# Performance work log

Hardware: AMD Instinct MI355X
Metric: run time of the kernel (lower is better)

## Reference

```python
import jax, jax.numpy as jnp
import numpy as np

D_MODEL = 1024
N_HEADS = 16
D_K = D_MODEL // N_HEADS
FF_DIM = 4096
EPS = 1e-6
NEG = -1.0e9


def _layernorm(x, g, b):
    # torch: a_2 * (x - mean) / (std + eps) + b_2, std is unbiased (ddof=1)
    mean = jnp.mean(x, axis=-1, keepdims=True)
    std = jnp.std(x, axis=-1, keepdims=True, ddof=1)
    return g * (x - mean) / (std + EPS) + b


def setup_inputs() -> dict:
    key = jax.random.key(0)
    ks = jax.random.split(key, 8)
    s = 0.02
    x = jax.random.normal(ks[0], (2, 2048, D_MODEL), dtype=jnp.float32)
    mask = jnp.ones((2, 1, 1, 2048), dtype=jnp.int32)
    return {
        "x": x,
        "mask": mask,
        "wq": jax.random.normal(ks[1], (D_MODEL, D_MODEL), jnp.float32) * s,
        "wk": jax.random.normal(ks[2], (D_MODEL, D_MODEL), jnp.float32) * s,
        "wv": jax.random.normal(ks[3], (D_MODEL, D_MODEL), jnp.float32) * s,
        "wo": jax.random.normal(ks[4], (D_MODEL, D_MODEL), jnp.float32) * s,
        "bq": jnp.zeros((D_MODEL,), jnp.float32),
        "bk": jnp.zeros((D_MODEL,), jnp.float32),
        "bv": jnp.zeros((D_MODEL,), jnp.float32),
        "bo": jnp.zeros((D_MODEL,), jnp.float32),
        "w1": jax.random.normal(ks[5], (D_MODEL, FF_DIM), jnp.float32) * s,
        "b1": jnp.zeros((FF_DIM,), jnp.float32),
        "w2": jax.random.normal(ks[6], (FF_DIM, D_MODEL), jnp.float32) * s,
        "b2": jnp.zeros((D_MODEL,), jnp.float32),
        "ln1_g": jnp.ones((D_MODEL,), jnp.float32),
        "ln1_b": jnp.zeros((D_MODEL,), jnp.float32),
        "ln2_g": jnp.ones((D_MODEL,), jnp.float32),
        "ln2_b": jnp.zeros((D_MODEL,), jnp.float32),
    }


def reference(x, mask, wq, wk, wv, wo, bq, bk, bv, bo, w1, b1, w2, b2,
              ln1_g, ln1_b, ln2_g, ln2_b):
    B, S, _ = x.shape
    # --- sublayer 1: pre-norm self-attention with residual ---
    h = _layernorm(x, ln1_g, ln1_b)
    q = (h @ wq + bq).reshape(B, S, N_HEADS, D_K).transpose(0, 2, 1, 3)
    k = (h @ wk + bk).reshape(B, S, N_HEADS, D_K).transpose(0, 2, 1, 3)
    v = (h @ wv + bv).reshape(B, S, N_HEADS, D_K).transpose(0, 2, 1, 3)
    scores = jnp.einsum('bhqd,bhkd->bhqk', q, k) / np.sqrt(D_K).astype(np.float32)
    scores = jnp.where(mask == 0, NEG, scores)
    attn = jax.nn.softmax(scores, axis=-1)
    ctx = jnp.einsum('bhqk,bhkd->bhqd', attn, v)
    ctx = ctx.transpose(0, 2, 1, 3).reshape(B, S, D_MODEL)
    x = x + (ctx @ wo + bo)
    # --- sublayer 2: pre-norm FFN with residual ---
    h2 = _layernorm(x, ln2_g, ln2_b)
    ff = jax.nn.relu(h2 @ w1 + b1) @ w2 + b2
    return x + ff
```

## Files before the change

### kernel.cpp

```cpp
#include <hip/hip_runtime.h>

typedef unsigned short u16;
typedef unsigned int u32;
typedef __attribute__((ext_vector_type(8))) short bf16x8;
typedef __attribute__((ext_vector_type(4))) float f32x4;

__device__ __forceinline__ u16 f2bf(float f) {
  union { float f; unsigned int u; } x;
  x.f = f;
  unsigned int r = x.u + 0x7fffu + ((x.u >> 16) & 1u);
  return (u16)(r >> 16);
}

__device__ __forceinline__ float bf2f(u16 v) {
  union { unsigned int u; float f; } x;
  x.u = ((unsigned int)v) << 16;
  return x.f;
}

__device__ __forceinline__ u32 fbits(float f) {
  union { float f; u32 u; } x; x.f = f; return x.u;
}

__device__ __forceinline__ void async16(const u16* g, u16* l) {
  __builtin_amdgcn_global_load_lds((const __attribute__((address_space(1))) void*)g,
                                   (__attribute__((address_space(3))) void*)l, 16, 0, 0);
}

__device__ __forceinline__ void stage128x64(const u16* __restrict__ src, long row0, int k0,
                                            int ld, u16* lds, int wave, int lane) {
#pragma unroll
  for (int r = 0; r < 4; ++r) {
    int s = r * 256 + wave * 64 + lane;
    int row = s >> 3;
    int c = (s & 7) ^ (row & 7);
    async16(src + (row0 + row) * (long)ld + k0 + c * 8, lds + (r * 256 + wave * 64) * 8);
  }
}

__device__ __forceinline__ void stage_half512(const u16* __restrict__ src, long row0, int k0,
                                              int ld, u16* lbase, int wave, int lane) {
#pragma unroll
  for (int r = 0; r < 2; ++r) {
    int s = r * 512 + wave * 64 + lane;
    int row = s >> 3;
    int c = (s & 7) ^ (row & 7);
    async16(src + (row0 + row) * (long)ld + k0 + c * 8, lbase + (r * 512 + wave * 64) * 8);
  }
}

__device__ __forceinline__ void stage64x128(const u16* __restrict__ src, int col0, int ld,
                                            u16* lds, int wave, int lane) {
#pragma unroll
  for (int r = 0; r < 4; ++r) {
    int s = r * 256 + wave * 64 + lane;
    int row = s >> 4;
    int c = (s & 15) ^ (row & 15);
    async16(src + (long)row * ld + col0 + c * 8, lds + (r * 256 + wave * 64) * 8);
  }
}

__device__ __forceinline__ void ln_core(float4 v, const float* g, const float* b, int t,
                                        u16* outrow) {
  float s = v.x + v.y + v.z + v.w;
  float ss = v.x * v.x + v.y * v.y + v.z * v.z + v.w * v.w;
#pragma unroll
  for (int off = 32; off; off >>= 1) {
    s += __shfl_xor(s, off);
    ss += __shfl_xor(ss, off);
  }
  __shared__ float red[8];
  int wave = t >> 6, lane = t & 63;
  if (lane == 0) { red[wave] = s; red[wave + 4] = ss; }
  __syncthreads();
  float tot = red[0] + red[1] + red[2] + red[3];
  float tots = red[4] + red[5] + red[6] + red[7];
  float mean = tot * (1.0f / 1024.0f);
  float var = (tots - 1024.0f * mean * mean) * (1.0f / 1023.0f);
  var = fmaxf(var, 0.0f);
  float inv = 1.0f / (sqrtf(var) + 1e-6f);
  float4 gv = ((const float4*)g)[t];
  float4 bv = ((const float4*)b)[t];
  union { unsigned long long u64; u16 h[4]; } o;
  o.h[0] = f2bf(gv.x * (v.x - mean) * inv + bv.x);
  o.h[1] = f2bf(gv.y * (v.y - mean) * inv + bv.y);
  o.h[2] = f2bf(gv.z * (v.z - mean) * inv + bv.z);
  o.h[3] = f2bf(gv.w * (v.w - mean) * inv + bv.w);
  *(unsigned long long*)(outrow + t * 4) = o.u64;
}

__global__ __launch_bounds__(256) void prep(const float* __restrict__ wq,
                                            const float* __restrict__ wk,
                                            const float* __restrict__ wv,
                                            const float* __restrict__ wo,
                                            const float* __restrict__ w1,
                                            const float* __restrict__ w2,
                                            const float* __restrict__ x,
                                            const float* __restrict__ ln1_g,
                                            const float* __restrict__ ln1_b,
                                            u16* __restrict__ wqkvT,
                                            u16* __restrict__ w1T,
                                            u16* __restrict__ w2T,
                                            u16* __restrict__ hout) {
  const int bid = blockIdx.x;
  const int part = bid >> 12;
  const int local = bid & 4095;
  const int t = threadIdx.x;
  if (part == 1) {
    float4 v = ((const float4*)(x + (long)local * 1024))[t];
    ln_core(v, ln1_g, ln1_b, t, hout + (long)local * 1024);
    return;
  }
  __shared__ float tile[32][33];
  const float* src; u16* dst; int C, R, bx, by;
  if (part == 0) {
    int sub = local >> 10;
    src = sub == 0 ? wq : (sub == 1 ? wk : (sub == 2 ? wv : wo));
    dst = wqkvT + (long)sub * 1024 * 1024;
    C = 1024; R = 1024; bx = local & 31; by = (local >> 5) & 31;
  } else if (part == 2) {
    src = w1; dst = w1T; C = 4096; R = 1024; bx = local & 127; by = local >> 7;
  } else {
    src = w2; dst = w2T; C = 1024; R = 4096; bx = local & 31; by = local >> 5;
  }
  int c0 = bx * 32, r0 = by * 32;
  int tx = t & 31, ty = t >> 5;
#pragma unroll
  for (int i = 0; i < 32; i += 8)
    tile[ty + i][tx] = src[(long)(r0 + ty + i) * C + c0 + tx];
  __syncthreads();
#pragma unroll
  for (int i = 0; i < 32; i += 8)
    dst[(long)(c0 + ty + i) * R + r0 + tx] = f2bf(tile[tx][ty + i]);
}

__global__ __launch_bounds__(256) void ln_fuse(const float* __restrict__ x,
                                               const float* __restrict__ bres,
                                               const u16* __restrict__ p0,
                                               const u16* __restrict__ p1,
                                               const float* __restrict__ g,
                                               const float* __restrict__ b,
                                               float* __restrict__ yout,
                                               u16* __restrict__ hout) {
  int row = blockIdx.x, t = threadIdx.x;
  long base = (long)row * 1024;
  float4 xv = ((const float4*)(x + base))[t];
  float4 bo = ((const float4*)bres)[t];
  ushort4 a = ((const ushort4*)(p0 + base))[t];
  ushort4 c = ((const ushort4*)(p1 + base))[t];
  float4 y;
  y.x = xv.x + bo.x + bf2f(a.x) + bf2f(c.x);
  y.y = xv.y + bo.y + bf2f(a.y) + bf2f(c.y);
  y.z = xv.z + bo.z + bf2f(a.z) + bf2f(c.z);
  y.w = xv.w + bo.w + bf2f(a.w) + bf2f(c.w);
  ((float4*)(yout + base))[t] = y;
  ln_core(y, g, b, t, hout + base);
}

__global__ __launch_bounds__(256) void final_add(float* __restrict__ out,
                                                 const float* __restrict__ b2,
                                                 const u16* __restrict__ p0,
                                                 const u16* __restrict__ p1,
                                                 const u16* __restrict__ p2,
                                                 const u16* __restrict__ p3) {
  int row = blockIdx.x, t = threadIdx.x;
  long base = (long)row * 1024;
  float4 o = ((float4*)(out + base))[t];
  float4 bb = ((const float4*)b2)[t];
  ushort4 a = ((const ushort4*)(p0 + base))[t];
  ushort4 c = ((const ushort4*)(p1 + base))[t];
  ushort4 d = ((const ushort4*)(p2 + base))[t];
  ushort4 e = ((const ushort4*)(p3 + base))[t];
  o.x += bb.x + (bf2f(a.x) + bf2f(c.x)) + (bf2f(d.x) + bf2f(e.x));
  o.y += bb.y + (bf2f(a.y) + bf2f(c.y)) + (bf2f(d.y) + bf2f(e.y));
  o.z += bb.z + (bf2f(a.z) + bf2f(c.z)) + (bf2f(d.z) + bf2f(e.z));
  o.w += bb.w + (bf2f(a.w) + bf2f(c.w)) + (bf2f(d.w) + bf2f(e.w));
  ((float4*)(out + base))[t] = o;
}

template <int MODE>
__global__ __launch_bounds__(256) void gemm_bt(const u16* __restrict__ A,
                                               const u16* __restrict__ Bt, int M, int N, int K,
                                               void* __restrict__ outp,
                                               const float* __restrict__ bias0,
                                               const float* __restrict__ bias1,
                                               const float* __restrict__ bias2,
                                               u16* __restrict__ q_out, u16* __restrict__ k_out,
                                               u16* __restrict__ v_out) {
  __shared__ __align__(16) u16 lds[17408];
  u16* ldsA = lds;
  u16* ldsB = lds + 8192;
  const int tid = threadIdx.x;
  const int wave = tid >> 6, lane = tid & 63;
  const int lane16 = lane & 15, quad = lane >> 4;
  const int wm = (wave >> 1) * 64, wn = (wave & 1) * 64;
  const long m0 = (long)blockIdx.y * 128;
  const long n0 = (long)blockIdx.x * 128;
  const int kLen = K / gridDim.z;
  const int kBeg = blockIdx.z * kLen;

  const f32x4 fzero = {0.f, 0.f, 0.f, 0.f};
  f32x4 acc[4][4];
#pragma unroll
  for (int i = 0; i < 4; ++i)
#pragma unroll
    for (int j = 0; j < 4; ++j) acc[i][j] = fzero;

  for (int k0 = kBeg; k0 < kBeg + kLen; k0 += 64) {
    stage128x64(A, m0, k0, K, ldsA, wave, lane);
    stage128x64(Bt, n0, k0, K, ldsB, wave, lane);
    __syncthreads();
#pragma unroll
    for (int kk = 0; kk < 2; ++kk) {
      bf16x8 af[4], bfr[4];
#pragma unroll
      for (int i = 0; i < 4; ++i) {
        int row = wm + i * 16 + lane16;
        int c = (kk * 4 + quad) ^ (row & 7);
        af[i] = *(const bf16x8*)(ldsA + row * 64 + c * 8);
      }
#pragma unroll
      for (int j = 0; j < 4; ++j) {
        int row = wn + j * 16 + lane16;
        int c = (kk * 4 + quad) ^ (row & 7);
        bfr[j] = *(const bf16x8*)(ldsB + row * 64 + c * 8);
      }
#pragma unroll
      for (int i = 0; i < 4; ++i)
#pragma unroll
        for (int j = 0; j < 4; ++j)
          acc[i][j] = __builtin_amdgcn_mfma_f32_16x16x32_bf16(af[i], bfr[j], acc[i][j], 0, 0, 0);
    }
    __syncthreads();
  }

  if (MODE == 0 && (int)(n0 >> 10) == 2) {
#pragma unroll
    for (int j = 0; j < 4; ++j) {
      int lcol = wn + j * 16 + lane16;
      float bvj = bias2[(int)(n0 - 2048) + lcol];
#pragma unroll
      for (int i = 0; i < 4; ++i)
#pragma unroll
        for (int r = 0; r < 4; ++r) {
          int lrow = wm + i * 16 + quad * 4 + r;
          lds[lcol * 136 + lrow] = f2bf(acc[i][j][r] + bvj);
        }
    }
    __syncthreads();
    int lcol = tid >> 1, seg = tid & 1;
    int cc = (int)(n0 - 2048) + lcol;
    int head = cc >> 6, d = cc & 63;
    int bI = (int)(m0 >> 11), s0 = (int)(m0 & 2047);
    u16* dst = v_out + ((long)(bI * 16 + head) * 64 + d) * 2048 + s0 + seg * 64;
    const u16* s = lds + lcol * 136 + seg * 64;
#pragma unroll
    for (int c2 = 0; c2 < 8; ++c2) ((uint4*)dst)[c2] = ((const uint4*)s)[c2];
    return;
  }

  u16* pp = nullptr;
  if (MODE == 1) pp = blockIdx.z == 0 ? (u16*)outp : q_out;

#pragma unroll
  for (int j = 0; j < 4; ++j) {
    int col = (int)n0 + wn + j * 16 + lane16;
#pragma unroll
    for (int i = 0; i < 4; ++i) {
#pragma unroll
      for (int r = 0; r < 4; ++r) {
        int row = (int)m0 + wm + i * 16 + quad * 4 + r;
        float val = acc[i][j][r];
        if (MODE == 0) {
          int which = col >> 10, cc = col & 1023;
          float vv = val + (which == 0 ? bias0[cc] : bias1[cc]);
          int bb = row >> 11, sS = row & 2047, head = cc >> 6, d = cc & 63;
          long bh = (long)bb * 16 + head;
          if (which == 0) {
            q_out[(bh * 2048 + sS) * 64 + d] = f2bf(vv * 0.18033688f);
          } else {
            k_out[(bh * 2048 + sS) * 64 + d] = f2bf(vv);
          }
        } else if (MODE == 1) {
          pp[(long)row * N + col] = f2bf(val);
        }
      }
    }
  }
}

template <int MODE>
__global__ __launch_bounds__(512, 1) void gemm8(const u16* __restrict__ A,
                                                const u16* __restrict__ Bt, int M, int N, int K,
                                                void* __restrict__ outp,
                                                const float* __restrict__ bias) {
  __shared__ __align__(16) u16 lds[65536];
  (void)M;
  const int tid = threadIdx.x;
  const int wave = tid >> 6, lane = tid & 63;
  const int lane16 = lane & 15, quad = lane >> 4;
  const int wr2 = wave >> 2, wc2 = wave & 3;
  const long m0 = (long)blockIdx.y * 256;
  const long n0 = (long)blockIdx.x * 256;
  const int kLen = K / gridDim.z;
  const int kBeg = blockIdx.z * kLen;
  const int nT = kLen >> 6;

  u16* const ldsA = lds;
  u16* const ldsB = lds + 32768;

  const f32x4 fzero = {0.f, 0.f, 0.f, 0.f};
  f32x4 acc[2][2][4][2];
#pragma unroll
  for (int qa = 0; qa < 2; ++qa)
#pragma unroll
    for (int qb = 0; qb < 2; ++qb)
#pragma unroll
      for (int m = 0; m < 4; ++m)
#pragma unroll
        for (int n = 0; n < 2; ++n) acc[qa][qb][m][n] = fzero;

  stage_half512(A,  m0,       kBeg,      K, ldsA,                 wave, lane);
  stage_half512(Bt, n0,       kBeg,      K, ldsB,                 wave, lane);
  stage_half512(Bt, n0 + 128, kBeg,      K, ldsB + 8192,          wave, lane);
  stage_half512(A,  m0 + 128, kBeg,      K, ldsA + 8192,          wave, lane);
  stage_half512(A,  m0,       kBeg + 64, K, ldsA + 16384,         wave, lane);
  stage_half512(Bt, n0,       kBeg + 64, K, ldsB + 16384,         wave, lane);
  stage_half512(Bt, n0 + 128, kBeg + 64, K, ldsB + 16384 + 8192,  wave, lane);
  asm volatile("s_waitcnt vmcnt(10)" ::: "memory");
  asm volatile("s_barrier" ::: "memory");

  for (int t = 0; t < nT; ++t) {
    u16* const aB = ldsA + (t & 1) * 16384;
    u16* const bB = ldsB + (t & 1) * 16384;
    u16* const aN1 = ldsA + ((t + 1) & 1) * 16384;
    const int k1 = kBeg + (t + 1 < nT ? t + 1 : nT - 1) * 64;
    const int k2 = kBeg + (t + 2 < nT ? t + 2 : nT - 1) * 64;

    bf16x8 af[4][2], b0f[2][2], b1f[2][2];

#pragma unroll
    for (int m = 0; m < 4; ++m) {
      const int row = wr2 * 64 + m * 16 + lane16;
#pragma unroll
      for (int kk = 0; kk < 2; ++kk)
        af[m][kk] = *(const bf16x8*)(aB + row * 64 + (((kk * 4 + quad) ^ (row & 7)) << 3));
    }
#pragma unroll
    for (int n = 0; n < 2; ++n) {
      const int row = wc2 * 32 + n * 16 + lane16;
#pragma unroll
      for (int kk = 0; kk < 2; ++kk)
        b0f[n][kk] = *(const bf16x8*)(bB + row * 64 + (((kk * 4 + quad) ^ (row & 7)) << 3));
    }
    stage_half512(A, m0 + 128, k1, K, aN1 + 8192, wave, lane);
    asm volatile("s_barrier" ::: "memory");
    asm volatile("s_waitcnt lgkmcnt(0)" ::: "memory");
    __builtin_amdgcn_sched_barrier(0);
    __builtin_amdgcn_s_setprio(1);
#pragma unroll
    for (int m = 0; m < 4; ++m)
#pragma unroll
      for (int n = 0; n < 2; ++n) {
        acc[0][0][m][n] = __builtin_amdgcn_mfma_f32_16x16x32_bf16(af[m][0], b0f[n][0], acc[0][0][m][n], 0, 0, 0);
        acc[0][0][m][n] = __builtin_amdgcn_mfma_f32_16x16x32_bf16(af[m][1], b0f[n][1], acc[0][0][m][n], 0, 0, 0);
      }
    __builtin_amdgcn_s_setprio(0);
    asm volatile("s_waitcnt vmcnt(10)" ::: "memory");
    asm volatile("s_barrier" ::: "memory");

#pragma unroll
    for (int n = 0; n < 2; ++n) {
      const int row = 128 + wc2 * 32 + n * 16 + lane16;
#pragma unroll
      for (int kk = 0; kk < 2; ++kk)
        b1f[n][kk] = *(const bf16x8*)(bB + row * 64 + (((kk * 4 + quad) ^ (row & 7)) << 3));
    }
    stage_half512(A, m0, k2, K, aB, wave, lane);
    asm volatile("s_barrier" ::: "memory");
    asm volatile("s_waitcnt lgkmcnt(0)" ::: "memory");
    __builtin_amdgcn_sched_barrier(0);
    __builtin_amdgcn_s_setprio(1);
#pragma unroll
    for (int m = 0; m < 4; ++m)
#pragma unroll
      for (int n = 0; n < 2; ++n) {
        acc[0][1][m][n] = __builtin_amdgcn_mfma_f32_16x16x32_bf16(af[m][0], b1f[n][0], acc[0][1][m][n], 0, 0, 0);
        acc[0][1][m][n] = __builtin_amdgcn_mfma_f32_16x16x32_bf16(af[m][1], b1f[n][1], acc[0][1][m][n], 0, 0, 0);
      }
    __builtin_amdgcn_s_setprio(0);
    asm volatile("s_waitcnt vmcnt(10)" ::: "memory");
    asm volatile("s_barrier" ::: "memory");

#pragma unroll
    for (int m = 0; m < 4; ++m) {
      const int row = 128 + wr2 * 64 + m * 16 + lane16;
#pragma unroll
      for (int kk = 0; kk < 2; ++kk)
        af[m][kk] = *(const bf16x8*)(aB + row * 64 + (((kk * 4 + quad) ^ (row & 7)) << 3));
    }
    stage_half512(Bt, n0, k2, K, bB, wave, lane);
    asm volatile("s_barrier" ::: "memory");
    asm volatile("s_waitcnt lgkmcnt(0)" ::: "memory");
    __builtin_amdgcn_sched_barrier(0);
    __builtin_amdgcn_s_setprio(1);
#pragma unroll
    for (int m = 0; m < 4; ++m)
#pragma unroll
      for (int n = 0; n < 2; ++n) {
        acc[1][1][m][n] = __builtin_amdgcn_mfma_f32_16x16x32_bf16(af[m][0], b1f[n][0], acc[1][1][m][n], 0, 0, 0);
        acc[1][1][m][n] = __builtin_amdgcn_mfma_f32_16x16x32_bf16(af[m][1], b1f[n][1], acc[1][1][m][n], 0, 0, 0);
      }
    __builtin_amdgcn_s_setprio(0);
    asm volatile("s_waitcnt vmcnt(10)" ::: "memory");
    asm volatile("s_barrier" ::: "memory");

    stage_half512(Bt, n0 + 128, k2, K, bB + 8192, wave, lane);
    asm volatile("s_barrier" ::: "memory");
    __builtin_amdgcn_s_setprio(1);
#pragma unroll
    for (int m = 0; m < 4; ++m)
#pragma unroll
      for (int n = 0; n < 2; ++n) {
        acc[1][0][m][n] = __builtin_amdgcn_mfma_f32_16x16x32_bf16(af[m][0], b0f[n][0], acc[1][0][m][n], 0, 0, 0);
        acc[1][0][m][n] = __builtin_amdgcn_mfma_f32_16x16x32_bf16(af[m][1], b0f[n][1], acc[1][0][m][n], 0, 0, 0);
      }
    __builtin_amdgcn_s_setprio(0);
    asm volatile("s_waitcnt vmcnt(10)" ::: "memory");
    asm volatile("s_barrier" ::: "memory");
  }

  asm volatile("s_waitcnt vmcnt(0)" ::: "memory");

  if (MODE == 2) {
    u16* op = (u16*)outp;
#pragma unroll
    for (int qa = 0; qa < 2; ++qa)
#pragma unroll
      for (int qb = 0; qb < 2; ++qb)
#pragma unroll
        for (int n = 0; n < 2; ++n) {
          const int col = (int)n0 + qb * 128 + wc2 * 32 + n * 16 + lane16;
          const float bv = bias[col];
#pragma unroll
          for (int m = 0; m < 4; ++m) {
            const long rbase = ((long)m0 + qa * 128 + wr2 * 64 + m * 16 + quad * 4) * N + col;
#pragma unroll
            for (int r = 0; r < 4; ++r)
              op[rbase + (long)r * N] = f2bf(fmaxf(acc[qa][qb][m][n][r] + bv, 0.0f));
          }
        }
  } else {
    u16* pp = (u16*)outp + (long)blockIdx.z * 4194304;
#pragma unroll
    for (int qa = 0; qa < 2; ++qa)
#pragma unroll
      for (int qb = 0; qb < 2; ++qb)
#pragma unroll
        for (int n = 0; n < 2; ++n) {
          const int col = (int)n0 + qb * 128 + wc2 * 32 + n * 16 + lane16;
#pragma unroll
          for (int m = 0; m < 4; ++m) {
            const long rbase = ((long)m0 + qa * 128 + wr2 * 64 + m * 16 + quad * 4) * N + col;
#pragma unroll
            for (int r = 0; r < 4; ++r)
              pp[rbase + (long)r * N] = f2bf(acc[qa][qb][m][n][r]);
          }
        }
  }
}

#define FA_C0 28.854239f
__global__ __launch_bounds__(256) void flash_attn(const u16* __restrict__ q,
                                                  const u16* __restrict__ k,
                                                  const u16* __restrict__ v,
                                                  const int* __restrict__ mask,
                                                  u16* __restrict__ ctx) {
  const int fid = blockIdx.y * 16 + blockIdx.x;
  const int xcd = fid & 7, slot = fid >> 3;
  const int bh = xcd * 4 + (slot >> 4);
  const int q0 = (slot & 15) * 128;
  const int b = bh >> 4, h = bh & 15;
  const int tid = threadIdx.x;
  const int wave = tid >> 6, lane = tid & 63;
  const int lane16 = lane & 15, quad = lane >> 4;

  const u16* qp = q + (long)bh * 2048 * 64;
  const u16* kp = k + (long)bh * 2048 * 64;
  const u16* vp = v + (long)bh * 64 * 2048;
  const int* mp = mask + b * 2048;

  __shared__ __align__(16) u16 ldsK[128 * 64];
  __shared__ __align__(16) u16 ldsVT[64 * 128];
  __shared__ __align__(16) u16 ldsP23[2 * 4096];
  __shared__ __align__(16) float ldsMask[128];
  __shared__ int ldsFlag[2];
  u16* myP = (wave < 2) ? (ldsK + wave * 4096) : (ldsP23 + (wave - 2) * 4096);

  bf16x8 qf[2][2];
#pragma unroll
  for (int g = 0; g < 2; ++g) {
    const long qrow = q0 + wave * 32 + g * 16 + lane16;
    qf[g][0] = *(const bf16x8*)(qp + qrow * 64 + quad * 8);
    qf[g][1] = *(const bf16x8*)(qp + qrow * 64 + 32 + quad * 8);
  }

  const f32x4 fzero = {0.f, 0.f, 0.f, 0.f};
  const f32x4 cC0 = {-FA_C0, -FA_C0, -FA_C0, -FA_C0};
  float l_loc[2] = {0.f, 0.f};
  f32x4 o_acc[2][4];
#pragma unroll
  for (int g = 0; g < 2; ++g)
#pragma unroll
    for (int j = 0; j < 4; ++j) o_acc[g][j] = fzero;

  const int xorm = (lane16 & 7) << 2;
  u16* const pw0 = myP + lane16 * 128;
  u16* const pw1 = myP + (16 + lane16) * 128;

  for (int kt = 0; kt < 2048; kt += 128) {
    stage128x64(kp, kt, 0, 64, ldsK, wave, lane);
    stage64x128(vp, kt, 2048, ldsVT, wave, lane);
    if (tid < 128) {
      int mv = mp[kt + tid];
      ldsMask[tid] = (mv == 0) ? -1.0e9f : 0.0f;
      unsigned long long bal = __ballot(mv != 0);
      if ((tid & 63) == 0) ldsFlag[tid >> 6] = (bal == ~0ull) ? 1 : 0;
    }
    __syncthreads();
    const bool allv = (ldsFlag[0] & ldsFlag[1]) != 0;

    f32x4 s_acc[8][2];
#pragma unroll
    for (int j = 0; j < 8; ++j) {
      int row = j * 16 + lane16;
      int c0i = quad ^ (row & 7);
      int c1i = (4 + quad) ^ (row & 7);
      bf16x8 kf0 = *(const bf16x8*)(ldsK + row * 64 + c0i * 8);
      bf16x8 kf1 = *(const bf16x8*)(ldsK + row * 64 + c1i * 8);
#pragma unroll
      for (int g = 0; g < 2; ++g) {
        f32x4 sa = __builtin_amdgcn_mfma_f32_16x16x32_bf16(kf0, qf[g][0], cC0, 0, 0, 0);
        sa = __builtin_amdgcn_mfma_f32_16x16x32_bf16(kf1, qf[g][1], sa, 0, 0, 0);
        s_acc[j][g] = sa;
      }
    }
    __syncthreads();

#pragma unroll
    for (int j = 0; j < 8; ++j) {
      int cw = ((4 * j + quad) ^ xorm) * 4;
#pragma unroll
      for (int g = 0; g < 2; ++g) {
        f32x4 sa = s_acc[j][g];
        if (!allv) {
          f32x4 mk = *(const f32x4*)(ldsMask + j * 16 + quad * 4);
          sa = sa + mk;
        }
        float p0 = __builtin_exp2f(sa[0]);
        float p1 = __builtin_exp2f(sa[1]);
        float p2 = __builtin_exp2f(sa[2]);
        float p3 = __builtin_exp2f(sa[3]);
        l_loc[g] += (p0 + p1) + (p2 + p3);
        uint2 pk;
        pk.x = __builtin_amdgcn_perm(fbits(p1), fbits(p0), 0x07060302u);
        pk.y = __builtin_amdgcn_perm(fbits(p3), fbits(p2), 0x07060302u);
        *(uint2*)((g ? pw1 : pw0) + cw) = pk;
      }
    }
#pragma unroll
    for (int kk = 0; kk < 4; ++kk) {
      int cr = ((8 * kk + 2 * quad) ^ xorm) * 4;
      bf16x8 pf0 = *(const bf16x8*)(pw0 + cr);
      bf16x8 pf1 = *(const bf16x8*)(pw1 + cr);
#pragma unroll
      for (int jj = 0; jj < 4; ++jj) {
        int row = jj * 16 + lane16;
        int cv = (kk * 4 + quad) ^ (row & 15);
        bf16x8 vf = *(const bf16x8*)(ldsVT + row * 128 + cv * 8);
        o_acc[0][jj] = __builtin_amdgcn_mfma_f32_16x16x32_bf16(pf0, vf, o_acc[0][jj], 0, 0, 0);
        o_acc[1][jj] = __builtin_amdgcn_mfma_f32_16x16x32_bf16(pf1, vf, o_acc[1][jj], 0, 0, 0);
      }
    }
    __syncthreads();
  }

  float lr[2][4];
#pragma unroll
  for (int g = 0; g < 2; ++g) {
    float l = l_loc[g];
#pragma unroll
    for (int off = 16; off < 64; off <<= 1) l += __shfl_xor(l, off);
    float linv = 1.0f / l;
#pragma unroll
    for (int r = 0; r < 4; ++r) lr[g][r] = __shfl(linv, quad * 4 + r);
  }

#pragma unroll
  for (int g = 0; g < 2; ++g)
#pragma unroll
    for (int jj = 0; jj < 4; ++jj)
#pragma unroll
      for (int r = 0; r < 4; ++r) {
        int sg = q0 + wave * 32 + g * 16 + quad * 4 + r;
        int d = jj * 16 + lane16;
        float val = o_acc[g][jj][r] * lr[g][r];
        ctx[((long)b * 2048 + sg) * 1024 + h * 64 + d] = f2bf(val);
      }
}

extern "C" void kernel_launch(void* const* d_in, const int* in_sizes, int n_in, void* d_out,
                              int out_size, void* d_ws, size_t ws_size, hipStream_t stream) {
  (void)in_sizes; (void)n_in; (void)out_size; (void)ws_size;
  const float* x  = (const float*)d_in[0];
  const int* mask = (const int*)d_in[1];
  const float* wq = (const float*)d_in[2];
  const float* wk = (const float*)d_in[3];
  const float* wv = (const float*)d_in[4];
  const float* wo = (const float*)d_in[5];
  const float* bq = (const float*)d_in[6];
  const float* bk = (const float*)d_in[7];
  const float* bv = (const float*)d_in[8];
  const float* bo = (const float*)d_in[9];
  const float* w1 = (const float*)d_in[10];
  const float* b1 = (const float*)d_in[11];
  const float* w2 = (const float*)d_in[12];
  const float* b2 = (const float*)d_in[13];
  const float* ln1_g = (const float*)d_in[14];
  const float* ln1_b = (const float*)d_in[15];
  const float* ln2_g = (const float*)d_in[16];
  const float* ln2_b = (const float*)d_in[17];
  float* out = (float*)d_out;

  u16* ws = (u16*)d_ws;
  u16* wqkvT = ws;
  u16* woT = wqkvT + 3072 * 1024;
  u16* w1T = woT + 1024 * 1024;
  u16* w2T = w1T + 4096 * 1024;
  u16* h   = w2T + 4096 * 1024;
  u16* qb  = h + 4096 * 1024;
  u16* kb  = qb + 4096 * 1024;
  u16* vb  = kb + 4096 * 1024;
  u16* ctx = vb + 4096 * 1024;
  u16* ffh = qb;
  u16* f2p = ws;

  prep<<<16384, 256, 0, stream>>>(wq, wk, wv, wo, w1, w2, x, ln1_g, ln1_b,
                                  wqkvT, w1T, w2T, h);

  gemm_bt<0><<<dim3(24, 32), 256, 0, stream>>>(h, wqkvT, 4096, 3072, 1024, nullptr, bq, bk, bv,
                                               qb, kb, vb);

  flash_attn<<<dim3(16, 32), 256, 0, stream>>>(qb, kb, vb, mask, ctx);

  gemm_bt<1><<<dim3(8, 32, 2), 256, 0, stream>>>(ctx, woT, 4096, 1024, 1024, qb, nullptr,
                                                 nullptr, nullptr, kb, nullptr, nullptr);

  ln_fuse<<<4096, 256, 0, stream>>>(x, bo, qb, kb, ln2_g, ln2_b, out, h);

  gemm8<2><<<dim3(16, 16), 512, 0, stream>>>(h, w1T, 4096, 4096, 1024, ffh, b1);

  gemm8<1><<<dim3(4, 16, 4), 512, 0, stream>>>(ffh, w2T, 4096, 1024, 4096, f2p, nullptr);

  final_add<<<4096, 256, 0, stream>>>(out, b2, f2p, f2p + 4194304, f2p + 2 * 4194304,
                                      f2p + 3 * 4194304);
}
```

Baseline: 355.8 us.

## Move QKV and Wo GEMMs to 256-tile kernel, add XCD swizzle and priorities

Removes the 128-tile gemm_bt kernel. The QKV projection, including its Q/K/V head-layout epilogue, and the output projection now run on the 512-thread 256x256 gemm8 kernel, with the output projection using 4-way split-K. An optional block-index swizzle spreads tiles across XCDs for the QKV and FFN1 GEMMs. The FFN2 kernel now atomically adds one split-K slice directly into the fp32 output, so final_add reads three partials instead of four. In flash attention, s_setprio raises wave priority around the MFMA phases. The workspace is reused more aggressively, including an in-place read and write of h in ln_fuse, which creates buffer-aliasing risk.

Measured after the change: 360.0 us (median of 2 runs). Within noise of the previous version (+1.2%).

```diff
diff --git a/kernel.cpp b/kernel.cpp
--- a/kernel.cpp
+++ b/kernel.cpp
@@ -134,25 +134,24 @@
     dst[(long)(c0 + ty + i) * R + r0 + tx] = f2bf(tile[tx][ty + i]);
 }
 
-__global__ __launch_bounds__(256) void ln_fuse(const float* __restrict__ x,
-                                               const float* __restrict__ bres,
-                                               const u16* __restrict__ p0,
-                                               const u16* __restrict__ p1,
-                                               const float* __restrict__ g,
-                                               const float* __restrict__ b,
-                                               float* __restrict__ yout,
-                                               u16* __restrict__ hout) {
+__global__ __launch_bounds__(256) void ln_fuse(const float* x, const float* bres,
+                                               const u16* p0, const u16* p1,
+                                               const u16* p2, const u16* p3,
+                                               const float* g, const float* b,
+                                               float* yout, u16* hout) {
   int row = blockIdx.x, t = threadIdx.x;
   long base = (long)row * 1024;
   float4 xv = ((const float4*)(x + base))[t];
   float4 bo = ((const float4*)bres)[t];
   ushort4 a = ((const ushort4*)(p0 + base))[t];
   ushort4 c = ((const ushort4*)(p1 + base))[t];
+  ushort4 d = ((const ushort4*)(p2 + base))[t];
+  ushort4 e = ((const ushort4*)(p3 + base))[t];
   float4 y;
-  y.x = xv.x + bo.x + bf2f(a.x) + bf2f(c.x);
-  y.y = xv.y + bo.y + bf2f(a.y) + bf2f(c.y);
-  y.z = xv.z + bo.z + bf2f(a.z) + bf2f(c.z);
-  y.w = xv.w + bo.w + bf2f(a.w) + bf2f(c.w);
+  y.x = xv.x + bo.x + (bf2f(a.x) + bf2f(c.x)) + (bf2f(d.x) + bf2f(e.x));
+  y.y = xv.y + bo.y + (bf2f(a.y) + bf2f(c.y)) + (bf2f(d.y) + bf2f(e.y));
+  y.z = xv.z + bo.z + (bf2f(a.z) + bf2f(c.z)) + (bf2f(d.z) + bf2f(e.z));
+  y.w = xv.w + bo.w + (bf2f(a.w) + bf2f(c.w)) + (bf2f(d.w) + bf2f(e.w));
   ((float4*)(yout + base))[t] = y;
   ln_core(y, g, b, t, hout + base);
 }
@@ -161,8 +160,7 @@
                                                  const float* __restrict__ b2,
                                                  const u16* __restrict__ p0,
                                                  const u16* __restrict__ p1,
-                                                 const u16* __restrict__ p2,
-                                                 const u16* __restrict__ p3) {
+                                                 const u16* __restrict__ p2) {
   int row = blockIdx.x, t = threadIdx.x;
   long base = (long)row * 1024;
   float4 o = ((float4*)(out + base))[t];
@@ -170,138 +168,38 @@
   ushort4 a = ((const ushort4*)(p0 + base))[t];
   ushort4 c = ((const ushort4*)(p1 + base))[t];
   ushort4 d = ((const ushort4*)(p2 + base))[t];
-  ushort4 e = ((const ushort4*)(p3 + base))[t];
-  o.x += bb.x + (bf2f(a.x) + bf2f(c.x)) + (bf2f(d.x) + bf2f(e.x));
-  o.y += bb.y + (bf2f(a.y) + bf2f(c.y)) + (bf2f(d.y) + bf2f(e.y));
-  o.z += bb.z + (bf2f(a.z) + bf2f(c.z)) + (bf2f(d.z) + bf2f(e.z));
-  o.w += bb.w + (bf2f(a.w) + bf2f(c.w)) + (bf2f(d.w) + bf2f(e.w));
+  o.x += bb.x + (bf2f(a.x) + bf2f(c.x)) + bf2f(d.x);
+  o.y += bb.y + (bf2f(a.y) + bf2f(c.y)) + bf2f(d.y);
+  o.z += bb.z + (bf2f(a.z) + bf2f(c.z)) + bf2f(d.z);
+  o.w += bb.w + (bf2f(a.w) + bf2f(c.w)) + bf2f(d.w);
   ((float4*)(out + base))[t] = o;
 }
 
-template <int MODE>
-__global__ __launch_bounds__(256) void gemm_bt(const u16* __restrict__ A,
-                                               const u16* __restrict__ Bt, int M, int N, int K,
-                                               void* __restrict__ outp,
-                                               const float* __restrict__ bias0,
-                                               const float* __restrict__ bias1,
-                                               const float* __restrict__ bias2,
-                                               u16* __restrict__ q_out, u16* __restrict__ k_out,
-                                               u16* __restrict__ v_out) {
-  __shared__ __align__(16) u16 lds[17408];
-  u16* ldsA = lds;
-  u16* ldsB = lds + 8192;
-  const int tid = threadIdx.x;
-  const int wave = tid >> 6, lane = tid & 63;
-  const int lane16 = lane & 15, quad = lane >> 4;
-  const int wm = (wave >> 1) * 64, wn = (wave & 1) * 64;
-  const long m0 = (long)blockIdx.y * 128;
-  const long n0 = (long)blockIdx.x * 128;
-  const int kLen = K / gridDim.z;
-  const int kBeg = blockIdx.z * kLen;
-
-  const f32x4 fzero = {0.f, 0.f, 0.f, 0.f};
-  f32x4 acc[4][4];
-#pragma unroll
-  for (int i = 0; i < 4; ++i)
-#pragma unroll
-    for (int j = 0; j < 4; ++j) acc[i][j] = fzero;
-
-  for (int k0 = kBeg; k0 < kBeg + kLen; k0 += 64) {
-    stage128x64(A, m0, k0, K, ldsA, wave, lane);
-    stage128x64(Bt, n0, k0, K, ldsB, wave, lane);
-    __syncthreads();
-#pragma unroll
-    for (int kk = 0; kk < 2; ++kk) {
-      bf16x8 af[4], bfr[4];
-#pragma unroll
-      for (int i = 0; i < 4; ++i) {
-        int row = wm + i * 16 + lane16;
-        int c = (kk * 4 + quad) ^ (row & 7);
-        af[i] = *(const bf16x8*)(ldsA + row * 64 + c * 8);
-      }
-#pragma unroll
-      for (int j = 0; j < 4; ++j) {
-        int row = wn + j * 16 + lane16;
-        int c = (kk * 4 + quad) ^ (row & 7);
-        bfr[j] = *(const bf16x8*)(ldsB + row * 64 + c * 8);
-      }
-#pragma unroll
-      for (int i = 0; i < 4; ++i)
-#pragma unroll
-        for (int j = 0; j < 4; ++j)
-          acc[i][j] = __builtin_amdgcn_mfma_f32_16x16x32_bf16(af[i], bfr[j], acc[i][j], 0, 0, 0);
-    }
-    __syncthreads();
-  }
-
-  if (MODE == 0 && (int)(n0 >> 10) == 2) {
-#pragma unroll
-    for (int j = 0; j < 4; ++j) {
-      int lcol = wn + j * 16 + lane16;
-      float bvj = bias2[(int)(n0 - 2048) + lcol];
-#pragma unroll
-      for (int i = 0; i < 4; ++i)
-#pragma unroll
-        for (int r = 0; r < 4; ++r) {
-          int lrow = wm + i * 16 + quad * 4 + r;
-          lds[lcol * 136 + lrow] = f2bf(acc[i][j][r] + bvj);
-        }
-    }
-    __syncthreads();
-    int lcol = tid >> 1, seg = tid & 1;
-    int cc = (int)(n0 - 2048) + lcol;
-    int head = cc >> 6, d = cc & 63;
-    int bI = (int)(m0 >> 11), s0 = (int)(m0 & 2047);
-    u16* dst = v_out + ((long)(bI * 16 + head) * 64 + d) * 2048 + s0 + seg * 64;
-    const u16* s = lds + lcol * 136 + seg * 64;
-#pragma unroll
-    for (int c2 = 0; c2 < 8; ++c2) ((uint4*)dst)[c2] = ((const uint4*)s)[c2];
-    return;
-  }
-
-  u16* pp = nullptr;
-  if (MODE == 1) pp = blockIdx.z == 0 ? (u16*)outp : q_out;
-
-#pragma unroll
-  for (int j = 0; j < 4; ++j) {
-    int col = (int)n0 + wn + j * 16 + lane16;
-#pragma unroll
-    for (int i = 0; i < 4; ++i) {
-#pragma unroll
-      for (int r = 0; r < 4; ++r) {
-        int row = (int)m0 + wm + i * 16 + quad * 4 + r;
-        float val = acc[i][j][r];
-        if (MODE == 0) {
-          int which = col >> 10, cc = col & 1023;
-          float vv = val + (which == 0 ? bias0[cc] : bias1[cc]);
-          int bb = row >> 11, sS = row & 2047, head = cc >> 6, d = cc & 63;
-          long bh = (long)bb * 16 + head;
-          if (which == 0) {
-            q_out[(bh * 2048 + sS) * 64 + d] = f2bf(vv * 0.18033688f);
-          } else {
-            k_out[(bh * 2048 + sS) * 64 + d] = f2bf(vv);
-          }
-        } else if (MODE == 1) {
-          pp[(long)row * N + col] = f2bf(val);
-        }
-      }
-    }
-  }
-}
-
-template <int MODE>
+template <int MODE, int SWZ>
 __global__ __launch_bounds__(512, 1) void gemm8(const u16* __restrict__ A,
                                                 const u16* __restrict__ Bt, int M, int N, int K,
                                                 void* __restrict__ outp,
-                                                const float* __restrict__ bias) {
+                                                const float* __restrict__ bias,
+                                                const float* __restrict__ bias1,
+                                                const float* __restrict__ bias2,
+                                                u16* __restrict__ q_out, u16* __restrict__ k_out,
+                                                u16* __restrict__ v_out) {
   __shared__ __align__(16) u16 lds[65536];
   (void)M;
   const int tid = threadIdx.x;
   const int wave = tid >> 6, lane = tid & 63;
   const int lane16 = lane & 15, quad = lane >> 4;
   const int wr2 = wave >> 2, wc2 = wave & 3;
-  const long m0 = (long)blockIdx.y * 256;
-  const long n0 = (long)blockIdx.x * 256;
+  int bx = blockIdx.x, by = blockIdx.y;
+  if (SWZ) {
+    const int fid = by * gridDim.x + bx;
+    const int xcd = fid & 7, slot = fid >> 3;
+    const int nxh = gridDim.x >> 1;
+    bx = (xcd & 1) * nxh + slot % nxh;
+    by = (xcd >> 1) * 4 + slot / nxh;
+  }
+  const long m0 = (long)by * 256;
+  const long n0 = (long)bx * 256;
   const int kLen = K / gridDim.z;
   const int kBeg = blockIdx.z * kLen;
   const int nT = kLen >> 6;
@@ -432,7 +330,66 @@
 
   asm volatile("s_waitcnt vmcnt(0)" ::: "memory");
 
-  if (MODE == 2) {
+  if (MODE == 0) {
+    const int sel = (int)(n0 >> 10);
+    if (sel == 2) {
+#pragma unroll
+      for (int qa = 0; qa < 2; ++qa)
+#pragma unroll
+        for (int qb = 0; qb < 2; ++qb) {
+          __syncthreads();
+#pragma unroll
+          for (int n = 0; n < 2; ++n) {
+            const int lcol = wc2 * 32 + n * 16 + lane16;
+            const float bvj = bias2[(int)(n0 - 2048) + qb * 128 + lcol];
+#pragma unroll
+            for (int m = 0; m < 4; ++m)
+#pragma unroll
+              for (int r = 0; r < 4; ++r) {
+                const int lrow = wr2 * 64 + m * 16 + quad * 4 + r;
+                lds[lcol * 136 + lrow] = f2bf(acc[qa][qb][m][n][r] + bvj);
+              }
+          }
+          __syncthreads();
+          const int lcol = tid >> 2, seg = tid & 3;
+          const int cc = (int)(n0 - 2048) + qb * 128 + lcol;
+          const int head = cc >> 6, d = cc & 63;
+          const int bI = (int)((m0 + qa * 128) >> 11);
+          const int s0 = (int)((m0 + qa * 128) & 2047);
+          u16* dst = v_out + ((long)(bI * 16 + head) * 64 + d) * 2048 + s0 + seg * 32;
+          const u16* s = lds + lcol * 136 + seg * 32;
+#pragma unroll
+          for (int c2 = 0; c2 < 4; ++c2) ((uint4*)dst)[c2] = ((const uint4*)s)[c2];
+        }
+      return;
+    }
+    u16* qk = sel == 0 ? q_out : k_out;
+    const float* bb = sel == 0 ? bias : bias1;
+#pragma unroll
+    for (int qa = 0; qa < 2; ++qa)
+#pragma unroll
+      for (int qb = 0; qb < 2; ++qb)
+#pragma unroll
+        for (int n = 0; n < 2; ++n) {
+          const int col = (int)n0 + qb * 128 + wc2 * 32 + n * 16 + lane16;
+          const int cc = col & 1023;
+          const float bv = bb[cc];
+          const int head = cc >> 6, d = cc & 63;
+#pragma unroll
+          for (int m = 0; m < 4; ++m) {
+            const int rw = (int)m0 + qa * 128 + wr2 * 64 + m * 16 + quad * 4;
+#pragma unroll
+            for (int r = 0; r < 4; ++r) {
+              const int row = rw + r;
+              const int bI = row >> 11, sS = row & 2047;
+              const long bh = (long)bI * 16 + head;
+              float vv = acc[qa][qb][m][n][r] + bv;
+              if (sel == 0) vv *= 0.18033688f;
+              qk[(bh * 2048 + sS) * 64 + d] = f2bf(vv);
+            }
+          }
+        }
+  } else if (MODE == 2) {
     u16* op = (u16*)outp;
 #pragma unroll
     for (int qa = 0; qa < 2; ++qa)
@@ -451,22 +408,42 @@
           }
         }
   } else {
-    u16* pp = (u16*)outp + (long)blockIdx.z * 4194304;
-#pragma unroll
-    for (int qa = 0; qa < 2; ++qa)
-#pragma unroll
-      for (int qb = 0; qb < 2; ++qb)
-#pragma unroll
-        for (int n = 0; n < 2; ++n) {
-          const int col = (int)n0 + qb * 128 + wc2 * 32 + n * 16 + lane16;
-#pragma unroll
-          for (int m = 0; m < 4; ++m) {
-            const long rbase = ((long)m0 + qa * 128 + wr2 * 64 + m * 16 + quad * 4) * N + col;
-#pragma unroll
-            for (int r = 0; r < 4; ++r)
-              pp[rbase + (long)r * N] = f2bf(acc[qa][qb][m][n][r]);
+    const int z = blockIdx.z;
+    if (MODE == 3 && z == 3) {
+      float* op = (float*)v_out;
+#pragma unroll
+      for (int qa = 0; qa < 2; ++qa)
+#pragma unroll
+        for (int qb = 0; qb < 2; ++qb)
+#pragma unroll
+          for (int n = 0; n < 2; ++n) {
+            const int col = (int)n0 + qb * 128 + wc2 * 32 + n * 16 + lane16;
+#pragma unroll
+            for (int m = 0; m < 4; ++m) {
+              const long rbase = ((long)m0 + qa * 128 + wr2 * 64 + m * 16 + quad * 4) * N + col;
+#pragma unroll
+              for (int r = 0; r < 4; ++r)
+                unsafeAtomicAdd(op + rbase + (long)r * N, acc[qa][qb][m][n][r]);
+            }
           }
-        }
+    } else {
+      u16* pp = z == 0 ? (u16*)outp : (z == 1 ? q_out : (z == 2 ? k_out : v_out));
+#pragma unroll
+      for (int qa = 0; qa < 2; ++qa)
+#pragma unroll
+        for (int qb = 0; qb < 2; ++qb)
+#pragma unroll
+          for (int n = 0; n < 2; ++n) {
+            const int col = (int)n0 + qb * 128 + wc2 * 32 + n * 16 + lane16;
+#pragma unroll
+            for (int m = 0; m < 4; ++m) {
+              const long rbase = ((long)m0 + qa * 128 + wr2 * 64 + m * 16 + quad * 4) * N + col;
+#pragma unroll
+              for (int r = 0; r < 4; ++r)
+                pp[rbase + (long)r * N] = f2bf(acc[qa][qb][m][n][r]);
+            }
+          }
+    }
   }
 }
 
@@ -531,6 +508,7 @@
     const bool allv = (ldsFlag[0] & ldsFlag[1]) != 0;
 
     f32x4 s_acc[8][2];
+    __builtin_amdgcn_s_setprio(1);
 #pragma unroll
     for (int j = 0; j < 8; ++j) {
       int row = j * 16 + lane16;
@@ -545,6 +523,7 @@
         s_acc[j][g] = sa;
       }
     }
+    __builtin_amdgcn_s_setprio(0);
     __syncthreads();
 
 #pragma unroll
@@ -568,6 +547,7 @@
         *(uint2*)((g ? pw1 : pw0) + cw) = pk;
       }
     }
+    __builtin_amdgcn_s_setprio(1);
 #pragma unroll
     for (int kk = 0; kk < 4; ++kk) {
       int cr = ((8 * kk + 2 * quad) ^ xorm) * 4;
@@ -582,6 +562,7 @@
         o_acc[1][jj] = __builtin_amdgcn_mfma_f32_16x16x32_bf16(pf1, vf, o_acc[1][jj], 0, 0, 0);
       }
     }
+    __builtin_amdgcn_s_setprio(0);
     __syncthreads();
   }
 
@@ -643,25 +624,25 @@
   u16* vb  = kb + 4096 * 1024;
   u16* ctx = vb + 4096 * 1024;
   u16* ffh = qb;
-  u16* f2p = ws;
 
   prep<<<16384, 256, 0, stream>>>(wq, wk, wv, wo, w1, w2, x, ln1_g, ln1_b,
                                   wqkvT, w1T, w2T, h);
 
-  gemm_bt<0><<<dim3(24, 32), 256, 0, stream>>>(h, wqkvT, 4096, 3072, 1024, nullptr, bq, bk, bv,
-                                               qb, kb, vb);
+  gemm8<0, 1><<<dim3(12, 16), 512, 0, stream>>>(h, wqkvT, 4096, 3072, 1024, nullptr,
+                                                bq, bk, bv, qb, kb, vb);
 
   flash_attn<<<dim3(16, 32), 256, 0, stream>>>(qb, kb, vb, mask, ctx);
 
-  gemm_bt<1><<<dim3(8, 32, 2), 256, 0, stream>>>(ctx, woT, 4096, 1024, 1024, qb, nullptr,
-                                                 nullptr, nullptr, kb, nullptr, nullptr);
-
-  ln_fuse<<<4096, 256, 0, stream>>>(x, bo, qb, kb, ln2_g, ln2_b, out, h);
-
-  gemm8<2><<<dim3(16, 16), 512, 0, stream>>>(h, w1T, 4096, 4096, 1024, ffh, b1);
-
-  gemm8<1><<<dim3(4, 16, 4), 512, 0, stream>>>(ffh, w2T, 4096, 1024, 4096, f2p, nullptr);
-
-  final_add<<<4096, 256, 0, stream>>>(out, b2, f2p, f2p + 4194304, f2p + 2 * 4194304,
-                                      f2p + 3 * 4194304);
-}
+  gemm8<1, 0><<<dim3(4, 16, 4), 512, 0, stream>>>(ctx, woT, 4096, 1024, 1024, h,
+                                                  nullptr, nullptr, nullptr, qb, kb, vb);
+
+  ln_fuse<<<4096, 256, 0, stream>>>(x, bo, h, qb, kb, vb, ln2_g, ln2_b, out, h);
+
+  gemm8<2, 1><<<dim3(16, 16), 512, 0, stream>>>(h, w1T, 4096, 4096, 1024, ffh, b1,
+                                                nullptr, nullptr, nullptr, nullptr, nullptr);
+
+  gemm8<3, 0><<<dim3(4, 16, 4), 512, 0, stream>>>(ffh, w2T, 4096, 1024, 4096, ws,
+                                                  nullptr, nullptr, nullptr, w1T, h, (u16*)out);
+
+  final_add<<<4096, 256, 0, stream>>>(out, b2, ws, w1T, h);
+}
```
